# Kernel optimization log

Hardware: AMD Instinct MI355X
Metric: run time of the kernel (lower is better)

The kernel has to match this reference:

```python
import jax, jax.numpy as jnp
import numpy as np

B, C, T_, H_, W_ = 8, 64, 64, 56, 56
E = 2 * C          # predictor embed dim
K = 8              # frames to select
NS = 500           # perturbation samples
SIGMA = 0.05
LN_EPS = 1e-5


def setup_inputs() -> dict:
    key = jax.random.key(0)
    ks = jax.random.split(key, 4)
    x = jax.random.normal(ks[0], (B, C, T_, H_, W_), dtype=jnp.float32)
    ln_w = jnp.ones((E,), jnp.float32)
    ln_b = jnp.zeros((E,), jnp.float32)
    w1 = jax.random.normal(ks[1], (E, E), jnp.float32) * 0.02
    b1 = jnp.zeros((E,), jnp.float32)
    w2 = jax.random.normal(ks[2], (E, 1), jnp.float32) * 0.02
    b2 = jnp.zeros((1,), jnp.float32)
    return {"x": x, "ln_w": ln_w, "ln_b": ln_b, "w1": w1, "b1": b1,
            "w2": w2, "b2": b2, "H": H_, "W": W_, "T": T_}


def _predictor(feat, ln_w, ln_b, w1, b1, w2, b2):
    # LayerNorm -> Linear -> GELU
    mu = feat.mean(-1, keepdims=True)
    var = ((feat - mu) ** 2).mean(-1, keepdims=True)
    h = (feat - mu) / jnp.sqrt(var + LN_EPS) * ln_w + ln_b
    h = jax.nn.gelu(h @ w1 + b1, approximate=False)          # [B,T,E]
    half = h.shape[-1] // 2
    local_x = h[..., :half]                                   # [B,T,E/2]
    global_x = h[..., half:].mean(axis=1, keepdims=True)      # [B,1,E/2]
    g = jnp.broadcast_to(global_x, local_x.shape)
    h = jnp.concatenate([local_x, g], axis=-1)                # [B,T,E]
    return jax.nn.gelu(h @ w2 + b2, approximate=False)        # [B,T,1]


def _min_max_norm(s):
    lo = s.min(-1, keepdims=True)
    hi = s.max(-1, keepdims=True)
    return (s - lo) / (hi - lo + 1e-5)


def _perturbed_topk_indicator(scores, noise):
    # scores [b,d], noise [b,ns,d] -> indicator [b,k,d]
    perturbed = scores[:, None, :] + noise * SIGMA
    _, idx = jax.lax.top_k(perturbed, K)          # [b,ns,k]
    idx = jnp.sort(idx, axis=-1)
    oh = jax.nn.one_hot(idx, scores.shape[-1], dtype=scores.dtype)  # [b,ns,k,d]
    return oh.mean(axis=1)                        # [b,k,d]


def reference(x, ln_w, ln_b, w1, b1, w2, b2, H, W, T):
    b = x.shape[0]
    c = x.shape[1]
    n = H * W
    # b c t h w -> b t (h w) c
    xt = jnp.transpose(x, (0, 2, 3, 4, 1)).reshape(b, T, n, c)
    avg = xt.mean(axis=2)                          # [B,T,C]
    mx = xt.max(axis=2)                            # [B,T,C]
    feat = jnp.concatenate([avg, mx], axis=-1)     # [B,T,2C]
    scores = _predictor(feat, ln_w, ln_b, w1, b1, w2, b2)[..., 0]  # [B,T]
    scores = _min_max_norm(scores)
    noise = jax.random.normal(jax.random.key(42), (b, NS, T), dtype=scores.dtype)
    indicator = _perturbed_topk_indicator(scores, noise)  # [B,K,T]
    xf = xt.reshape(b, T, n * c)                   # flatten as (h w c)
    patches = jnp.einsum('bkt,btm->bkm', indicator, xf)   # [B,K,N*C]
    # b k (h w c) -> b c k h w
    patches = patches.reshape(b, K, H, W, c).transpose(0, 4, 1, 2, 3)
    return patches
```

## Files before the change

kernel.cpp:

```cpp
#include <hip/hip_runtime.h>
#include <math.h>

#define B_  8
#define C_  64
#define T_  64
#define HW_ 3136
#define E_  128
#define K_  8
#define NS_ 500

__global__ __launch_bounds__(256) void k_reduce(const float* __restrict__ x,
                                                float* __restrict__ feat) {
    int u  = blockIdx.x;
    int t  = u & 63;
    int bc = u >> 6;
    int c  = bc & 63;
    int b  = bc >> 6;
    const float4* p = (const float4*)(x + (size_t)u * HW_);
    float s = 0.f, m = -INFINITY;
    for (int i = threadIdx.x; i < HW_ / 4; i += 256) {
        float4 v = p[i];
        s += v.x + v.y + v.z + v.w;
        m = fmaxf(m, fmaxf(fmaxf(v.x, v.y), fmaxf(v.z, v.w)));
    }
    for (int o = 32; o; o >>= 1) {
        s += __shfl_down(s, o);
        m = fmaxf(m, __shfl_down(m, o));
    }
    __shared__ float ss[4], sm[4];
    int wid = threadIdx.x >> 6, lane = threadIdx.x & 63;
    if (lane == 0) { ss[wid] = s; sm[wid] = m; }
    __syncthreads();
    if (threadIdx.x == 0) {
        s = ss[0] + ss[1] + ss[2] + ss[3];
        m = fmaxf(fmaxf(sm[0], sm[1]), fmaxf(sm[2], sm[3]));
        float* fr = feat + (size_t)(b * T_ + t) * E_;
        fr[c]      = s / 3136.0f;
        fr[C_ + c] = m;
    }
}

__global__ __launch_bounds__(128) void k_mlp1(const float* __restrict__ feat,
                                              const float* __restrict__ ln_w,
                                              const float* __restrict__ ln_b,
                                              const float* __restrict__ w1,
                                              const float* __restrict__ b1,
                                              float* __restrict__ h) {
    int r = blockIdx.x;
    int j = threadIdx.x;
    __shared__ float nr[E_];
    __shared__ float red[2];
    float f = feat[(size_t)r * E_ + j];
    float s = f;
    for (int o = 32; o; o >>= 1) s += __shfl_down(s, o);
    if ((j & 63) == 0) red[j >> 6] = s;
    __syncthreads();
    float mu = (red[0] + red[1]) * (1.0f / 128.0f);
    __syncthreads();
    float d = f - mu;
    s = d * d;
    for (int o = 32; o; o >>= 1) s += __shfl_down(s, o);
    if ((j & 63) == 0) red[j >> 6] = s;
    __syncthreads();
    float var = (red[0] + red[1]) * (1.0f / 128.0f);
    float n = d / sqrtf(var + 1e-5f) * ln_w[j] + ln_b[j];
    nr[j] = n;
    __syncthreads();
    float acc = b1[j];
    #pragma unroll 8
    for (int i = 0; i < E_; i++) acc = fmaf(nr[i], w1[i * E_ + j], acc);
    float g = 0.5f * acc * (1.0f + erff(acc * 0.70710678118654752f));
    h[(size_t)r * E_ + j] = g;
}

__global__ __launch_bounds__(256) void k_score(const float* __restrict__ h,
                                               const float* __restrict__ w2,
                                               const float* __restrict__ b2,
                                               float* __restrict__ scores,
                                               float* __restrict__ ind) {
    int b = blockIdx.x;
    int tid = threadIdx.x;
    __shared__ float gm[64];
    __shared__ float sv[64];
    __shared__ float gdot_s, lo_s, hi_s;
    ind[b * 512 + tid]       = 0.f;
    ind[b * 512 + 256 + tid] = 0.f;
    if (tid < 64) {
        float s = 0.f;
        for (int t = 0; t < T_; t++)
            s += h[(size_t)(b * T_ + t) * E_ + 64 + tid];
        gm[tid] = s * (1.0f / 64.0f);
    }
    __syncthreads();
    if (tid < 64) {
        float s = gm[tid] * w2[64 + tid];
        for (int o = 32; o; o >>= 1) s += __shfl_down(s, o);
        if (tid == 0) gdot_s = s;
    }
    __syncthreads();
    if (tid < 64) {
        int t = tid;
        float acc = 0.f;
        for (int i = 0; i < 64; i++)
            acc = fmaf(h[(size_t)(b * T_ + t) * E_ + i], w2[i], acc);
        float pre = acc + gdot_s + b2[0];
        sv[t] = 0.5f * pre * (1.0f + erff(pre * 0.70710678118654752f));
    }
    __syncthreads();
    if (tid < 64) {
        float v = sv[tid];
        float mn = v, mx = v;
        for (int o = 32; o; o >>= 1) {
            mn = fminf(mn, __shfl_down(mn, o));
            mx = fmaxf(mx, __shfl_down(mx, o));
        }
        if (tid == 0) { lo_s = mn; hi_s = mx; }
    }
    __syncthreads();
    if (tid < 64)
        scores[b * T_ + tid] = (sv[tid] - lo_s) / (hi_s - lo_s + 1e-5f);
}

__device__ inline float jax_normal(unsigned idx) {
    unsigned x0 = 0u;
    unsigned x1 = idx;
    const unsigned k0 = 0u, k1 = 42u;
    const unsigned k2 = 0x1BD11BDAu ^ k0 ^ k1;
    x0 += k0; x1 += k1;
#define R_(r) { x0 += x1; x1 = (x1 << r) | (x1 >> (32 - r)); x1 ^= x0; }
    R_(13) R_(15) R_(26) R_(6)
    x0 += k1; x1 += k2 + 1u;
    R_(17) R_(29) R_(16) R_(24)
    x0 += k2; x1 += k0 + 2u;
    R_(13) R_(15) R_(26) R_(6)
    x0 += k0; x1 += k1 + 3u;
    R_(17) R_(29) R_(16) R_(24)
    x0 += k1; x1 += k2 + 4u;
    R_(13) R_(15) R_(26) R_(6)
    x0 += k2; x1 += k0 + 5u;
#undef R_
    unsigned bits = x0 ^ x1;
    float f = __uint_as_float((bits >> 9) | 0x3F800000u) - 1.0f;
    const float lo = -0.99999994f;
    float u = f * 2.0f + lo;
    u = fmaxf(lo, u);
    float w = -log1pf(-u * u);
    float p;
    if (w < 5.0f) {
        w -= 2.5f;
        p = 2.81022636e-08f;
        p = fmaf(p, w, 3.43273939e-07f);
        p = fmaf(p, w, -3.5233877e-06f);
        p = fmaf(p, w, -4.39150654e-06f);
        p = fmaf(p, w, 0.00021858087f);
        p = fmaf(p, w, -0.00125372503f);
        p = fmaf(p, w, -0.00417768164f);
        p = fmaf(p, w, 0.246640727f);
        p = fmaf(p, w, 1.50140941f);
    } else {
        w = sqrtf(w) - 3.0f;
        p = -0.000200214257f;
        p = fmaf(p, w, 0.000100950558f);
        p = fmaf(p, w, 0.00134934322f);
        p = fmaf(p, w, -0.00367342844f);
        p = fmaf(p, w, 0.00573950773f);
        p = fmaf(p, w, -0.0076224613f);
        p = fmaf(p, w, 0.00943887047f);
        p = fmaf(p, w, 1.00167406f);
        p = fmaf(p, w, 2.83297682f);
    }
    return 1.41421356237f * (p * u);
}

__global__ __launch_bounds__(64) void k_topk(const float* __restrict__ scores,
                                             float* __restrict__ ind) {
    int bs = blockIdx.x;
    int t  = threadIdx.x;
    int b  = bs / NS_;
    float nrm = jax_normal((unsigned)(bs * 64 + t));
    float v = scores[b * 64 + t] + nrm * 0.05f;
    __shared__ float pv[64];
    pv[t] = v;
    __syncthreads();
    int rank = 0;
    for (int j = 0; j < 64; j++) {
        float o = pv[j];
        rank += (o > v) || (o == v && j < t);
    }
    bool sel = rank < K_;
    unsigned long long m = __ballot(sel);
    if (sel) {
        int pos = __popcll(m & ((1ull << t) - 1ull));
        atomicAdd(&ind[b * 512 + pos * 64 + t], 1.0f);
    }
}

__global__ __launch_bounds__(256) void k_einsum(const float* __restrict__ x,
                                                const float* __restrict__ ind,
                                                float* __restrict__ out) {
    int gid   = blockIdx.x * 256 + threadIdx.x;
    int plane = gid / 784;
    int i     = gid - plane * 784;
    int b     = plane >> 6;
    int tid   = threadIdx.x;
    __shared__ float w[K_ * T_];
    __shared__ float wsum[T_];
    w[tid]       = ind[b * 512 + tid]       / 500.0f;
    w[tid + 256] = ind[b * 512 + 256 + tid] / 500.0f;
    __syncthreads();
    if (tid < 64) {
        float s = 0.f;
        #pragma unroll
        for (int k = 0; k < K_; k++) s += w[k * 64 + tid];
        wsum[tid] = s;
    }
    __syncthreads();

    const float4* xp = (const float4*)x + (size_t)plane * (T_ * 784) + i;
    float4 acc[K_];
    #pragma unroll
    for (int k = 0; k < K_; k++) acc[k] = make_float4(0.f, 0.f, 0.f, 0.f);

    for (int t = 0; t < T_; t++) {
        if (wsum[t] != 0.f) {
            float4 v = xp[(size_t)t * 784];
            #pragma unroll
            for (int k = 0; k < K_; k++) {
                float wk = w[k * 64 + t];
                acc[k].x = fmaf(wk, v.x, acc[k].x);
                acc[k].y = fmaf(wk, v.y, acc[k].y);
                acc[k].z = fmaf(wk, v.z, acc[k].z);
                acc[k].w = fmaf(wk, v.w, acc[k].w);
            }
        }
    }
    float4* op = (float4*)out + (size_t)plane * (K_ * 784) + i;
    #pragma unroll
    for (int k = 0; k < K_; k++) op[(size_t)k * 784] = acc[k];
}

extern "C" void kernel_launch(void* const* d_in, const int* in_sizes, int n_in,
                              void* d_out, int out_size, void* d_ws, size_t ws_size,
                              hipStream_t stream) {
    (void)in_sizes; (void)n_in; (void)out_size; (void)ws_size;
    const float* x    = (const float*)d_in[0];
    const float* ln_w = (const float*)d_in[1];
    const float* ln_b = (const float*)d_in[2];
    const float* w1   = (const float*)d_in[3];
    const float* b1   = (const float*)d_in[4];
    const float* w2   = (const float*)d_in[5];
    const float* b2   = (const float*)d_in[6];
    float* out = (float*)d_out;
    float* ws  = (float*)d_ws;
    float* feat   = ws;
    float* h      = ws + 65536;
    float* scores = ws + 131072;
    float* ind    = ws + 131584;

    hipLaunchKernelGGL(k_reduce, dim3(B_ * C_ * T_), dim3(256), 0, stream, x, feat);
    hipLaunchKernelGGL(k_mlp1,   dim3(B_ * T_),      dim3(128), 0, stream,
                       feat, ln_w, ln_b, w1, b1, h);
    hipLaunchKernelGGL(k_score,  dim3(B_),           dim3(256), 0, stream,
                       h, w2, b2, scores, ind);
    hipLaunchKernelGGL(k_topk,   dim3(B_ * NS_),     dim3(64),  0, stream, scores, ind);
    hipLaunchKernelGGL(k_einsum, dim3(1568),         dim3(256), 0, stream, x, ind, out);
}
```

Before: 129.7 us.

## Fuse MLP, scoring and perturbed top-k into one per-batch kernel

Replaces the separate MLP, score and top-k kernels with a single kernel per batch element that keeps hidden activations and scores in shared memory and counts top-k selections with shared-memory integer atomics. This removes two kernel launches, global intermediate traffic and global atomics. In exchange, the middle stage now runs on only eight blocks, serializing the 500 perturbation samples across 16 wavefronts per batch.

```diff
diff --git a/kernel.cpp b/kernel.cpp
--- a/kernel.cpp
+++ b/kernel.cpp
@@ -38,87 +38,6 @@
         fr[c]      = s / 3136.0f;
         fr[C_ + c] = m;
     }
-}
-
-__global__ __launch_bounds__(128) void k_mlp1(const float* __restrict__ feat,
-                                              const float* __restrict__ ln_w,
-                                              const float* __restrict__ ln_b,
-                                              const float* __restrict__ w1,
-                                              const float* __restrict__ b1,
-                                              float* __restrict__ h) {
-    int r = blockIdx.x;
-    int j = threadIdx.x;
-    __shared__ float nr[E_];
-    __shared__ float red[2];
-    float f = feat[(size_t)r * E_ + j];
-    float s = f;
-    for (int o = 32; o; o >>= 1) s += __shfl_down(s, o);
-    if ((j & 63) == 0) red[j >> 6] = s;
-    __syncthreads();
-    float mu = (red[0] + red[1]) * (1.0f / 128.0f);
-    __syncthreads();
-    float d = f - mu;
-    s = d * d;
-    for (int o = 32; o; o >>= 1) s += __shfl_down(s, o);
-    if ((j & 63) == 0) red[j >> 6] = s;
-    __syncthreads();
-    float var = (red[0] + red[1]) * (1.0f / 128.0f);
-    float n = d / sqrtf(var + 1e-5f) * ln_w[j] + ln_b[j];
-    nr[j] = n;
-    __syncthreads();
-    float acc = b1[j];
-    #pragma unroll 8
-    for (int i = 0; i < E_; i++) acc = fmaf(nr[i], w1[i * E_ + j], acc);
-    float g = 0.5f * acc * (1.0f + erff(acc * 0.70710678118654752f));
-    h[(size_t)r * E_ + j] = g;
-}
-
-__global__ __launch_bounds__(256) void k_score(const float* __restrict__ h,
-                                               const float* __restrict__ w2,
-                                               const float* __restrict__ b2,
-                                               float* __restrict__ scores,
-                                               float* __restrict__ ind) {
-    int b = blockIdx.x;
-    int tid = threadIdx.x;
-    __shared__ float gm[64];
-    __shared__ float sv[64];
-    __shared__ float gdot_s, lo_s, hi_s;
-    ind[b * 512 + tid]       = 0.f;
-    ind[b * 512 + 256 + tid] = 0.f;
-    if (tid < 64) {
-        float s = 0.f;
-        for (int t = 0; t < T_; t++)
-            s += h[(size_t)(b * T_ + t) * E_ + 64 + tid];
-        gm[tid] = s * (1.0f / 64.0f);
-    }
-    __syncthreads();
-    if (tid < 64) {
-        float s = gm[tid] * w2[64 + tid];
-        for (int o = 32; o; o >>= 1) s += __shfl_down(s, o);
-        if (tid == 0) gdot_s = s;
-    }
-    __syncthreads();
-    if (tid < 64) {
-        int t = tid;
-        float acc = 0.f;
-        for (int i = 0; i < 64; i++)
-            acc = fmaf(h[(size_t)(b * T_ + t) * E_ + i], w2[i], acc);
-        float pre = acc + gdot_s + b2[0];
-        sv[t] = 0.5f * pre * (1.0f + erff(pre * 0.70710678118654752f));
-    }
-    __syncthreads();
-    if (tid < 64) {
-        float v = sv[tid];
-        float mn = v, mx = v;
-        for (int o = 32; o; o >>= 1) {
-            mn = fminf(mn, __shfl_down(mn, o));
-            mx = fmaxf(mx, __shfl_down(mx, o));
-        }
-        if (tid == 0) { lo_s = mn; hi_s = mx; }
-    }
-    __syncthreads();
-    if (tid < 64)
-        scores[b * T_ + tid] = (sv[tid] - lo_s) / (hi_s - lo_s + 1e-5f);
 }
 
 __device__ inline float jax_normal(unsigned idx) {
@@ -172,27 +91,106 @@
     return 1.41421356237f * (p * u);
 }
 
-__global__ __launch_bounds__(64) void k_topk(const float* __restrict__ scores,
-                                             float* __restrict__ ind) {
-    int bs = blockIdx.x;
-    int t  = threadIdx.x;
-    int b  = bs / NS_;
-    float nrm = jax_normal((unsigned)(bs * 64 + t));
-    float v = scores[b * 64 + t] + nrm * 0.05f;
-    __shared__ float pv[64];
-    pv[t] = v;
-    __syncthreads();
-    int rank = 0;
-    for (int j = 0; j < 64; j++) {
-        float o = pv[j];
-        rank += (o > v) || (o == v && j < t);
-    }
-    bool sel = rank < K_;
-    unsigned long long m = __ballot(sel);
-    if (sel) {
-        int pos = __popcll(m & ((1ull << t) - 1ull));
-        atomicAdd(&ind[b * 512 + pos * 64 + t], 1.0f);
-    }
+#define HS_ 129
+__global__ __launch_bounds__(1024) void k_mid(const float* __restrict__ feat,
+                                              const float* __restrict__ ln_w,
+                                              const float* __restrict__ ln_b,
+                                              const float* __restrict__ w1,
+                                              const float* __restrict__ b1,
+                                              const float* __restrict__ w2,
+                                              const float* __restrict__ b2,
+                                              float* __restrict__ ind) {
+    int b    = blockIdx.x;
+    int tid  = threadIdx.x;
+    int wid  = tid >> 6;
+    int lane = tid & 63;
+    __shared__ float h_sh[T_ * HS_];
+    __shared__ float gm[64];
+    __shared__ float sc_sh[64];
+    __shared__ float gdot_sh;
+    __shared__ int   cnt[K_ * T_];
+
+    if (tid < 512) cnt[tid] = 0;
+
+    #pragma unroll
+    for (int q = 0; q < 4; q++) {
+        int t = wid * 4 + q;
+        const float* fr = feat + (size_t)(b * T_ + t) * E_;
+        float f0 = fr[lane], f1 = fr[lane + 64];
+        float s = f0 + f1;
+        for (int o = 32; o; o >>= 1) s += __shfl_xor(s, o);
+        float mu = s * (1.0f / 128.0f);
+        float d0 = f0 - mu, d1 = f1 - mu;
+        float s2 = d0 * d0 + d1 * d1;
+        for (int o = 32; o; o >>= 1) s2 += __shfl_xor(s2, o);
+        float rstd = 1.0f / sqrtf(s2 * (1.0f / 128.0f) + 1e-5f);
+        float n0 = d0 * rstd * ln_w[lane]      + ln_b[lane];
+        float n1 = d1 * rstd * ln_w[lane + 64] + ln_b[lane + 64];
+        float a0 = b1[lane], a1 = b1[lane + 64];
+        for (int i = 0; i < 64; i++) {
+            float ni = __shfl(n0, i);
+            a0 = fmaf(ni, w1[i * E_ + lane],      a0);
+            a1 = fmaf(ni, w1[i * E_ + 64 + lane], a1);
+        }
+        for (int i = 0; i < 64; i++) {
+            float ni = __shfl(n1, i);
+            a0 = fmaf(ni, w1[(64 + i) * E_ + lane],      a0);
+            a1 = fmaf(ni, w1[(64 + i) * E_ + 64 + lane], a1);
+        }
+        h_sh[t * HS_ + lane]      = 0.5f * a0 * (1.0f + erff(a0 * 0.70710678118654752f));
+        h_sh[t * HS_ + 64 + lane] = 0.5f * a1 * (1.0f + erff(a1 * 0.70710678118654752f));
+    }
+    __syncthreads();
+
+    if (tid < 64) {
+        float s = 0.f;
+        for (int t = 0; t < T_; t++) s += h_sh[t * HS_ + 64 + tid];
+        gm[tid] = s * (1.0f / 64.0f);
+    }
+    __syncthreads();
+    if (wid == 0) {
+        float s = gm[lane] * w2[64 + lane];
+        for (int o = 32; o; o >>= 1) s += __shfl_xor(s, o);
+        if (lane == 0) gdot_sh = s;
+    }
+    __syncthreads();
+    if (tid < 64) {
+        float acc = 0.f;
+        for (int i = 0; i < 64; i++)
+            acc = fmaf(h_sh[tid * HS_ + i], w2[i], acc);
+        float pre = acc + gdot_sh + b2[0];
+        sc_sh[tid] = 0.5f * pre * (1.0f + erff(pre * 0.70710678118654752f));
+    }
+    __syncthreads();
+    if (wid == 0) {
+        float v = sc_sh[lane];
+        float mn = v, mx = v;
+        for (int o = 32; o; o >>= 1) {
+            mn = fminf(mn, __shfl_xor(mn, o));
+            mx = fmaxf(mx, __shfl_xor(mx, o));
+        }
+        sc_sh[lane] = (v - mn) / (mx - mn + 1e-5f);
+    }
+    __syncthreads();
+
+    float myscore = sc_sh[lane];
+    for (int s = wid; s < NS_; s += 16) {
+        float nrm = jax_normal((unsigned)((b * NS_ + s) * 64 + lane));
+        float v = myscore + nrm * 0.05f;
+        int rank = 0;
+        for (int j = 0; j < 64; j++) {
+            float o = __shfl(v, j);
+            rank += (o > v) || (o == v && j < lane);
+        }
+        bool sel = rank < K_;
+        unsigned long long m = __ballot(sel);
+        if (sel) {
+            int pos = __popcll(m & ((1ull << lane) - 1ull));
+            atomicAdd(&cnt[pos * 64 + lane], 1);
+        }
+    }
+    __syncthreads();
+    if (tid < 512) ind[b * 512 + tid] = (float)cnt[tid];
 }
 
 __global__ __launch_bounds__(256) void k_einsum(const float* __restrict__ x,
@@ -252,16 +250,11 @@
     const float* b2   = (const float*)d_in[6];
     float* out = (float*)d_out;
     float* ws  = (float*)d_ws;
-    float* feat   = ws;
-    float* h      = ws + 65536;
-    float* scores = ws + 131072;
-    float* ind    = ws + 131584;
-
-    hipLaunchKernelGGL(k_reduce, dim3(B_ * C_ * T_), dim3(256), 0, stream, x, feat);
-    hipLaunchKernelGGL(k_mlp1,   dim3(B_ * T_),      dim3(128), 0, stream,
-                       feat, ln_w, ln_b, w1, b1, h);
-    hipLaunchKernelGGL(k_score,  dim3(B_),           dim3(256), 0, stream,
-                       h, w2, b2, scores, ind);
-    hipLaunchKernelGGL(k_topk,   dim3(B_ * NS_),     dim3(64),  0, stream, scores, ind);
-    hipLaunchKernelGGL(k_einsum, dim3(1568),         dim3(256), 0, stream, x, ind, out);
-}
+    float* feat = ws;
+    float* ind  = ws + 65536;
+
+    hipLaunchKernelGGL(k_reduce, dim3(B_ * C_ * T_), dim3(256),  0, stream, x, feat);
+    hipLaunchKernelGGL(k_mid,    dim3(B_),           dim3(1024), 0, stream,
+                       feat, ln_w, ln_b, w1, b1, w2, b2, ind);
+    hipLaunchKernelGGL(k_einsum, dim3(1568),         dim3(256),  0, stream, x, ind, out);
+}
```

New measurement: 261.9 us. +101.9%, slower.

## Fuse score computation into top-k kernel and reverse reduce block order

Applied to the files above, without the earlier changes.

Removes the separate scoring kernel: each top-k block now recomputes the per-batch scores redundantly, and the block handles four samples per 256-thread block, ranking with wave shuffles instead of shared memory. Indicator zeroing moves into the MLP kernel. The reduce kernel walks blocks in reverse order so the last-read parts of x are more likely still in cache when the einsum kernel reads x again. The aim is to save one launch and the serial gap between kernels, at the cost of recomputing the scores in every block.

```diff
diff --git a/kernel.cpp b/kernel.cpp
--- a/kernel.cpp
+++ b/kernel.cpp
@@ -11,7 +11,7 @@
 
 __global__ __launch_bounds__(256) void k_reduce(const float* __restrict__ x,
                                                 float* __restrict__ feat) {
-    int u  = blockIdx.x;
+    int u  = (B_ * C_ * T_ - 1) - blockIdx.x;
     int t  = u & 63;
     int bc = u >> 6;
     int c  = bc & 63;
@@ -45,9 +45,11 @@
                                               const float* __restrict__ ln_b,
                                               const float* __restrict__ w1,
                                               const float* __restrict__ b1,
-                                              float* __restrict__ h) {
+                                              float* __restrict__ h,
+                                              float* __restrict__ ind) {
     int r = blockIdx.x;
     int j = threadIdx.x;
+    if (r < 32) ind[r * 128 + j] = 0.f;
     __shared__ float nr[E_];
     __shared__ float red[2];
     float f = feat[(size_t)r * E_ + j];
@@ -71,54 +73,6 @@
     for (int i = 0; i < E_; i++) acc = fmaf(nr[i], w1[i * E_ + j], acc);
     float g = 0.5f * acc * (1.0f + erff(acc * 0.70710678118654752f));
     h[(size_t)r * E_ + j] = g;
-}
-
-__global__ __launch_bounds__(256) void k_score(const float* __restrict__ h,
-                                               const float* __restrict__ w2,
-                                               const float* __restrict__ b2,
-                                               float* __restrict__ scores,
-                                               float* __restrict__ ind) {
-    int b = blockIdx.x;
-    int tid = threadIdx.x;
-    __shared__ float gm[64];
-    __shared__ float sv[64];
-    __shared__ float gdot_s, lo_s, hi_s;
-    ind[b * 512 + tid]       = 0.f;
-    ind[b * 512 + 256 + tid] = 0.f;
-    if (tid < 64) {
-        float s = 0.f;
-        for (int t = 0; t < T_; t++)
-            s += h[(size_t)(b * T_ + t) * E_ + 64 + tid];
-        gm[tid] = s * (1.0f / 64.0f);
-    }
-    __syncthreads();
-    if (tid < 64) {
-        float s = gm[tid] * w2[64 + tid];
-        for (int o = 32; o; o >>= 1) s += __shfl_down(s, o);
-        if (tid == 0) gdot_s = s;
-    }
-    __syncthreads();
-    if (tid < 64) {
-        int t = tid;
-        float acc = 0.f;
-        for (int i = 0; i < 64; i++)
-            acc = fmaf(h[(size_t)(b * T_ + t) * E_ + i], w2[i], acc);
-        float pre = acc + gdot_s + b2[0];
-        sv[t] = 0.5f * pre * (1.0f + erff(pre * 0.70710678118654752f));
-    }
-    __syncthreads();
-    if (tid < 64) {
-        float v = sv[tid];
-        float mn = v, mx = v;
-        for (int o = 32; o; o >>= 1) {
-            mn = fminf(mn, __shfl_down(mn, o));
-            mx = fmaxf(mx, __shfl_down(mx, o));
-        }
-        if (tid == 0) { lo_s = mn; hi_s = mx; }
-    }
-    __syncthreads();
-    if (tid < 64)
-        scores[b * T_ + tid] = (sv[tid] - lo_s) / (hi_s - lo_s + 1e-5f);
 }
 
 __device__ inline float jax_normal(unsigned idx) {
@@ -172,26 +126,66 @@
     return 1.41421356237f * (p * u);
 }
 
-__global__ __launch_bounds__(64) void k_topk(const float* __restrict__ scores,
-                                             float* __restrict__ ind) {
-    int bs = blockIdx.x;
-    int t  = threadIdx.x;
-    int b  = bs / NS_;
-    float nrm = jax_normal((unsigned)(bs * 64 + t));
-    float v = scores[b * 64 + t] + nrm * 0.05f;
-    __shared__ float pv[64];
-    pv[t] = v;
-    __syncthreads();
+__global__ __launch_bounds__(256) void k_topk(const float* __restrict__ h,
+                                              const float* __restrict__ w2,
+                                              const float* __restrict__ b2,
+                                              float* __restrict__ ind) {
+    int blk  = blockIdx.x;
+    int b    = blk / 125;
+    int loc  = blk - b * 125;
+    int tid  = threadIdx.x;
+    int wid  = tid >> 6;
+    int lane = tid & 63;
+    __shared__ float gm[64];
+    __shared__ float sv[64];
+    __shared__ float gdot_s, lo_s, hi_s;
+    const float* hb = h + (size_t)b * T_ * E_;
+
+    if (tid < 64) {
+        float s = 0.f;
+        for (int t = 0; t < T_; t++) s += hb[t * E_ + 64 + tid];
+        gm[tid] = s * (1.0f / 64.0f);
+    }
+    __syncthreads();
+    if (wid == 0) {
+        float s = gm[lane] * w2[64 + lane];
+        for (int o = 32; o; o >>= 1) s += __shfl_down(s, o);
+        if (lane == 0) gdot_s = s;
+    }
+    __syncthreads();
+    if (tid < 64) {
+        float acc = 0.f;
+        for (int i = 0; i < 64; i++)
+            acc = fmaf(hb[tid * E_ + i], w2[i], acc);
+        float pre = acc + gdot_s + b2[0];
+        sv[tid] = 0.5f * pre * (1.0f + erff(pre * 0.70710678118654752f));
+    }
+    __syncthreads();
+    if (wid == 0) {
+        float v = sv[lane];
+        float mn = v, mx = v;
+        for (int o = 32; o; o >>= 1) {
+            mn = fminf(mn, __shfl_down(mn, o));
+            mx = fmaxf(mx, __shfl_down(mx, o));
+        }
+        if (lane == 0) { lo_s = mn; hi_s = mx; }
+    }
+    __syncthreads();
+    float myscore = (sv[lane] - lo_s) / (hi_s - lo_s + 1e-5f);
+
+    int s = loc * 4 + wid;
+    float nrm = jax_normal((unsigned)((b * NS_ + s) * 64 + lane));
+    float v = myscore + nrm * 0.05f;
     int rank = 0;
     for (int j = 0; j < 64; j++) {
-        float o = pv[j];
-        rank += (o > v) || (o == v && j < t);
+        float o = __shfl(v, j);
+        rank += (o > v) || (o == v && j < lane);
     }
     bool sel = rank < K_;
     unsigned long long m = __ballot(sel);
     if (sel) {
-        int pos = __popcll(m & ((1ull << t) - 1ull));
-        atomicAdd(&ind[b * 512 + pos * 64 + t], 1.0f);
+        int pos = __popcll(m & ((1ull << lane) - 1ull));
+        atomicAdd(&ind[b * 512 + pos * 64 + lane], 1.0f);
     }
 }
 
@@ -252,16 +246,14 @@
     const float* b2   = (const float*)d_in[6];
     float* out = (float*)d_out;
     float* ws  = (float*)d_ws;
-    float* feat   = ws;
-    float* h      = ws + 65536;
-    float* scores = ws + 131072;
-    float* ind    = ws + 131584;
+    float* feat = ws;
+    float* h    = ws + 65536;
+    float* ind  = ws + 131072;
 
     hipLaunchKernelGGL(k_reduce, dim3(B_ * C_ * T_), dim3(256), 0, stream, x, feat);
     hipLaunchKernelGGL(k_mlp1,   dim3(B_ * T_),      dim3(128), 0, stream,
-                       feat, ln_w, ln_b, w1, b1, h);
-    hipLaunchKernelGGL(k_score,  dim3(B_),           dim3(256), 0, stream,
-                       h, w2, b2, scores, ind);
-    hipLaunchKernelGGL(k_topk,   dim3(B_ * NS_),     dim3(64),  0, stream, scores, ind);
+                       feat, ln_w, ln_b, w1, b1, h, ind);
+    hipLaunchKernelGGL(k_topk,   dim3(B_ * 125),     dim3(256), 0, stream,
+                       h, w2, b2, ind);
     hipLaunchKernelGGL(k_einsum, dim3(1568),         dim3(256), 0, stream, x, ind, out);
 }
```

Result: no change. 129.7 us (-0.0%).
